# Performance work log

Hardware: AMD Instinct MI355X
Metric: run time of the kernel (lower is better)

Reference implementation:

```python
import jax, jax.numpy as jnp
import numpy as np

K = 1024  # attention hidden dim
H = 1024  # encoder hidden dim


def setup_inputs() -> dict:
    key = jax.random.key(0)
    ks = jax.random.split(key, 8)
    B, S = 32, 2048
    decoder_state = jax.random.normal(ks[0], (B, H), dtype=jnp.float32)
    encoder_hiddens = jax.random.normal(ks[1], (B, S, H), dtype=jnp.float32)
    # Linear params (torch convention: y = x @ W.T + b)
    Wa_w = jax.random.normal(ks[2], (1, K), dtype=jnp.float32) / np.sqrt(K)
    Wa_b = jnp.zeros((1,), dtype=jnp.float32)
    Wb_w = jax.random.normal(ks[3], (K, H), dtype=jnp.float32) / np.sqrt(H)
    Wb_b = jnp.zeros((K,), dtype=jnp.float32)
    Wc_w = jax.random.normal(ks[4], (K, H), dtype=jnp.float32) / np.sqrt(H)
    Wc_b = jnp.zeros((K,), dtype=jnp.float32)
    return {
        "decoder_state": decoder_state,
        "encoder_hiddens": encoder_hiddens,
        "Wa_w": Wa_w, "Wa_b": Wa_b,
        "Wb_w": Wb_w, "Wb_b": Wb_b,
        "Wc_w": Wc_w, "Wc_b": Wc_b,
    }


def reference(decoder_state, encoder_hiddens, Wa_w, Wa_b, Wb_w, Wb_b, Wc_w, Wc_b):
    # dec_proj: [B, K]; enc_proj: [B, S, K]
    dec_proj = decoder_state @ Wb_w.T + Wb_b
    enc_proj = jnp.einsum('bsh,kh->bsk', encoder_hiddens, Wc_w) + Wc_b
    # additive score: tanh then project to scalar -> [B, S]
    e = jnp.tanh(dec_proj[:, None, :] + enc_proj)
    scores = jnp.einsum('bsk,k->bs', e, Wa_w[0]) + Wa_b[0]
    attn = jax.nn.softmax(scores, axis=1)
    # weighted sum over sequence -> [B, H]
    context = jnp.einsum('bs,bsh->bh', attn, encoder_hiddens)
    return context
```

## Files before the change

### kernel.cpp

```cpp
#include <hip/hip_runtime.h>
#include <hip/hip_bf16.h>
#include <stdint.h>

#define B_SZ 32
#define S_SZ 2048
#define H_SZ 1024
#define K_SZ 1024
#define M_SZ (B_SZ * S_SZ)

typedef __attribute__((ext_vector_type(8))) short bf16x8;
typedef __attribute__((ext_vector_type(4))) float f32x4;


__device__ __forceinline__ short f2bf_rne(float f) {
    uint32_t u = __builtin_bit_cast(uint32_t, f);
    u += 0x7fffu + ((u >> 16) & 1u);
    return (short)(u >> 16);
}

__device__ __forceinline__ float bf2f(unsigned short u) {
    return __builtin_bit_cast(float, (uint32_t)u << 16);
}

__device__ __forceinline__ float fast_tanh(float x) {
    float ex = __expf(2.0f * x);
    return 1.0f - 2.0f / (ex + 1.0f);
}


__global__ void cvt_bf16_k(const float* __restrict__ in,
                           __hip_bfloat16* __restrict__ out, int n8) {
    int idx = blockIdx.x * blockDim.x + threadIdx.x;
    int stride = gridDim.x * blockDim.x;
    for (int i = idx; i < n8; i += stride) {
        const float4* p = (const float4*)in + (size_t)i * 2;
        float4 a = p[0], b = p[1];
        bf16x8 r;
        r[0] = f2bf_rne(a.x); r[1] = f2bf_rne(a.y);
        r[2] = f2bf_rne(a.z); r[3] = f2bf_rne(a.w);
        r[4] = f2bf_rne(b.x); r[5] = f2bf_rne(b.y);
        r[6] = f2bf_rne(b.z); r[7] = f2bf_rne(b.w);
        ((bf16x8*)out)[i] = r;
    }
}


__global__ __launch_bounds__(256) void decproj_k(
    const float* __restrict__ ds, const float* __restrict__ Wb,
    const float* __restrict__ Wb_b, const float* __restrict__ Wc_b,
    float* __restrict__ dp) {
    int g = blockIdx.x * 4 + (threadIdx.x >> 6);
    int lane = threadIdx.x & 63;
    int b = g >> 10;
    int k = g & 1023;
    const float4* wrow = (const float4*)(Wb + (size_t)k * H_SZ);
    const float4* xrow = (const float4*)(ds + (size_t)b * H_SZ);
    float sum = 0.f;
#pragma unroll
    for (int it = 0; it < 4; it++) {
        float4 w = wrow[lane + it * 64];
        float4 x = xrow[lane + it * 64];
        sum += w.x * x.x + w.y * x.y + w.z * x.z + w.w * x.w;
    }
#pragma unroll
    for (int off = 1; off < 64; off <<= 1) sum += __shfl_xor(sum, off, 64);
    if (lane == 0) dp[g] = sum + Wb_b[k] + Wc_b[k];
}


template <bool AF32>
__global__ __launch_bounds__(256) void gemm_scores_k(
    const void* __restrict__ Aptr, const __hip_bfloat16* __restrict__ Bw,
    const float* __restrict__ decp, const float* __restrict__ Wa,
    float* __restrict__ sp) {
    constexpr int ABYTES = AF32 ? 128 * 32 * 4 : 128 * 32 * 2;
    __shared__ __align__(16) unsigned char AsmRaw[ABYTES];
    __shared__ __align__(16) unsigned char BsmRaw[128 * 32 * 2];

    const int t = threadIdx.x;
    const int wave = t >> 6;
    const int lane = t & 63;
    const int wm = wave >> 1, wn = wave & 1;
    const int quad = lane >> 4;
    const int l15 = lane & 15;

    const int id = blockIdx.x;
    const int colBlk = (id >> 3) & 7;
    const int rowBlk = ((id >> 6) << 3) | (id & 7);
    const int row0 = rowBlk * 128;
    const int col0 = colBlk * 128;
    const int b = row0 >> 11;

    f32x4 acc[4][4];
#pragma unroll
    for (int i = 0; i < 4; i++)
#pragma unroll
        for (int j = 0; j < 4; j++) acc[i][j] = f32x4{0.f, 0.f, 0.f, 0.f};

    const __hip_bfloat16* Ab = (const __hip_bfloat16*)Aptr;
    const float* Af = (const float*)Aptr;

    for (int k0 = 0; k0 < H_SZ; k0 += 32) {
        if constexpr (AF32) {
#pragma unroll
            for (int inst = 0; inst < 4; inst++) {
                int slot = inst * 256 + t;
                int r = slot >> 3, c4 = slot & 7;
                const float* g = Af + (size_t)(row0 + r) * H_SZ + k0 + c4 * 4;
                __builtin_amdgcn_global_load_lds(
                    (const __attribute__((address_space(1))) void*)g,
                    (__attribute__((address_space(3))) void*)(AsmRaw + inst * 4096 + wave * 1024),
                    16, 0, 0);
            }
        } else {
#pragma unroll
            for (int inst = 0; inst < 2; inst++) {
                int slot = inst * 256 + t;
                int r = slot >> 2, c8 = slot & 3;
                const __hip_bfloat16* g = Ab + (size_t)(row0 + r) * H_SZ + k0 + c8 * 8;
                __builtin_amdgcn_global_load_lds(
                    (const __attribute__((address_space(1))) void*)g,
                    (__attribute__((address_space(3))) void*)(AsmRaw + inst * 4096 + wave * 1024),
                    16, 0, 0);
            }
        }
#pragma unroll
        for (int inst = 0; inst < 2; inst++) {
            int slot = inst * 256 + t;
            int r = slot >> 2, c8 = slot & 3;
            const __hip_bfloat16* g = Bw + (size_t)(col0 + r) * H_SZ + k0 + c8 * 8;
            __builtin_amdgcn_global_load_lds(
                (const __attribute__((address_space(1))) void*)g,
                (__attribute__((address_space(3))) void*)(BsmRaw + inst * 4096 + wave * 1024),
                16, 0, 0);
        }
        __syncthreads();

        bf16x8 afr[4], bfr[4];
#pragma unroll
        for (int i = 0; i < 4; i++) {
            int r = wm * 64 + i * 16 + l15;
            if constexpr (AF32) {
                const float* ap = (const float*)AsmRaw + r * 32 + quad * 8;
                f32x4 lo = *(const f32x4*)ap;
                f32x4 hi = *(const f32x4*)(ap + 4);
                bf16x8 v;
                v[0] = f2bf_rne(lo[0]); v[1] = f2bf_rne(lo[1]);
                v[2] = f2bf_rne(lo[2]); v[3] = f2bf_rne(lo[3]);
                v[4] = f2bf_rne(hi[0]); v[5] = f2bf_rne(hi[1]);
                v[6] = f2bf_rne(hi[2]); v[7] = f2bf_rne(hi[3]);
                afr[i] = v;
            } else {
                afr[i] = *(const bf16x8*)((const __hip_bfloat16*)AsmRaw + r * 32 + quad * 8);
            }
        }
#pragma unroll
        for (int j = 0; j < 4; j++) {
            int r = wn * 64 + j * 16 + l15;
            bfr[j] = *(const bf16x8*)((const __hip_bfloat16*)BsmRaw + r * 32 + quad * 8);
        }
#pragma unroll
        for (int i = 0; i < 4; i++)
#pragma unroll
            for (int j = 0; j < 4; j++)
                acc[i][j] = __builtin_amdgcn_mfma_f32_16x16x32_bf16(afr[i], bfr[j], acc[i][j], 0, 0, 0);
        __syncthreads();
    }

    float wa_j[4], dp_j[4];
#pragma unroll
    for (int j = 0; j < 4; j++) {
        int c = col0 + wn * 64 + j * 16 + l15;
        wa_j[j] = Wa[c];
        dp_j[j] = decp[b * K_SZ + c];
    }
    const int slotIdx = colBlk * 2 + wn;
#pragma unroll
    for (int i = 0; i < 4; i++) {
#pragma unroll
        for (int r = 0; r < 4; r++) {
            float tsum = 0.f;
#pragma unroll
            for (int j = 0; j < 4; j++)
                tsum += wa_j[j] * fast_tanh(acc[i][j][r] + dp_j[j]);
#pragma unroll
            for (int off = 1; off < 16; off <<= 1) tsum += __shfl_xor(tsum, off, 64);
            if (l15 == 0) {
                int m = row0 + wm * 64 + i * 16 + quad * 4 + r;
                sp[(size_t)slotIdx * M_SZ + m] = tsum;
            }
        }
    }
}


__global__ __launch_bounds__(256) void softmax_k(
    const float* __restrict__ sp, float* __restrict__ attn) {
    int b = blockIdx.x;
    int t = threadIdx.x;
    __shared__ float wred[4];
    __shared__ float wred2[4];
    float sc[8];
    float mx = -1e30f;
#pragma unroll
    for (int u = 0; u < 8; u++) {
        int m = b * S_SZ + t + u * 256;
        float v = 0.f;
#pragma unroll
        for (int c = 0; c < 16; c++) v += sp[(size_t)c * M_SZ + m];
        sc[u] = v;
        mx = fmaxf(mx, v);
    }
#pragma unroll
    for (int off = 1; off < 64; off <<= 1) mx = fmaxf(mx, __shfl_xor(mx, off, 64));
    if ((t & 63) == 0) wred[t >> 6] = mx;
    __syncthreads();
    mx = fmaxf(fmaxf(wred[0], wred[1]), fmaxf(wred[2], wred[3]));
    float lsum = 0.f;
#pragma unroll
    for (int u = 0; u < 8; u++) { sc[u] = expf(sc[u] - mx); lsum += sc[u]; }
#pragma unroll
    for (int off = 1; off < 64; off <<= 1) lsum += __shfl_xor(lsum, off, 64);
    if ((t & 63) == 0) wred2[t >> 6] = lsum;
    __syncthreads();
    float inv = 1.f / (wred2[0] + wred2[1] + wred2[2] + wred2[3]);
#pragma unroll
    for (int u = 0; u < 8; u++) attn[b * S_SZ + t + u * 256] = sc[u] * inv;
}


template <bool BF16E>
__global__ __launch_bounds__(256) void ctx_part_k(
    const float* __restrict__ attn, const void* __restrict__ encp,
    float* __restrict__ cp) {
    int b = blockIdx.x >> 5;
    int c = blockIdx.x & 31;
    int t = threadIdx.x;
    __shared__ float wloc[64];
    if (t < 64) wloc[t] = attn[b * S_SZ + c * 64 + t];
    __syncthreads();
    float4 acc = {0.f, 0.f, 0.f, 0.f};
    if constexpr (BF16E) {
        const ushort4* ep = (const ushort4*)((const __hip_bfloat16*)encp +
                              ((size_t)b * S_SZ + (size_t)c * 64) * H_SZ);
#pragma unroll 8
        for (int s = 0; s < 64; s++) {
            float w = wloc[s];
            ushort4 v = ep[s * 256 + t];
            acc.x += w * bf2f(v.x); acc.y += w * bf2f(v.y);
            acc.z += w * bf2f(v.z); acc.w += w * bf2f(v.w);
        }
    } else {
        const float4* ep = (const float4*)((const float*)encp +
                              ((size_t)b * S_SZ + (size_t)c * 64) * H_SZ);
#pragma unroll 8
        for (int s = 0; s < 64; s++) {
            float w = wloc[s];
            float4 v = ep[s * 256 + t];
            acc.x += w * v.x; acc.y += w * v.y;
            acc.z += w * v.z; acc.w += w * v.w;
        }
    }
    ((float4*)(cp + ((size_t)c * B_SZ + b) * H_SZ))[t] = acc;
}

__global__ void ctx_red_k(const float* __restrict__ cp, float* __restrict__ out) {
    int i = blockIdx.x * blockDim.x + threadIdx.x;
    float s = 0.f;
#pragma unroll
    for (int c = 0; c < 32; c++) s += cp[(size_t)c * (B_SZ * H_SZ) + i];
    out[i] = s;
}


extern "C" void kernel_launch(void* const* d_in, const int* in_sizes, int n_in,
                              void* d_out, int out_size, void* d_ws, size_t ws_size,
                              hipStream_t stream) {
    const float* dec  = (const float*)d_in[0];
    const float* enc  = (const float*)d_in[1];
    const float* Wa_w = (const float*)d_in[2];
    const float* Wb_w = (const float*)d_in[4];
    const float* Wb_b = (const float*)d_in[5];
    const float* Wc_w = (const float*)d_in[6];
    const float* Wc_b = (const float*)d_in[7];
    float* out = (float*)d_out;

    char* ws = (char*)d_ws;
    size_t off = 0;
    auto alloc = [&](size_t bytes) -> void* {
        void* p = ws + off;
        off += (bytes + 255) & ~(size_t)255;
        return p;
    };
    __hip_bfloat16* wc_bf = (__hip_bfloat16*)alloc((size_t)K_SZ * H_SZ * 2);
    float* dp     = (float*)alloc((size_t)B_SZ * K_SZ * 4);
    float* spart  = (float*)alloc((size_t)16 * M_SZ * 4);
    float* attn   = (float*)alloc((size_t)B_SZ * S_SZ * 4);
    float* cpart  = (float*)alloc((size_t)32 * B_SZ * H_SZ * 4);
    __hip_bfloat16* enc_bf = (__hip_bfloat16*)alloc((size_t)M_SZ * H_SZ * 2);
    const bool useBf16A = (off <= ws_size);

    cvt_bf16_k<<<512, 256, 0, stream>>>(Wc_w, wc_bf, K_SZ * H_SZ / 8);
    if (useBf16A)
        cvt_bf16_k<<<8192, 256, 0, stream>>>(enc, enc_bf, M_SZ * H_SZ / 8);
    decproj_k<<<8192, 256, 0, stream>>>(dec, Wb_w, Wb_b, Wc_b, dp);
    if (useBf16A)
        gemm_scores_k<false><<<(M_SZ / 128) * 8, 256, 0, stream>>>(enc_bf, wc_bf, dp, Wa_w, spart);
    else
        gemm_scores_k<true><<<(M_SZ / 128) * 8, 256, 0, stream>>>(enc, wc_bf, dp, Wa_w, spart);
    softmax_k<<<B_SZ, 256, 0, stream>>>(spart, attn);
    if (useBf16A)
        ctx_part_k<true><<<B_SZ * 32, 256, 0, stream>>>(attn, enc_bf, cpart);
    else
        ctx_part_k<false><<<B_SZ * 32, 256, 0, stream>>>(attn, enc, cpart);
    ctx_red_k<<<128, 256, 0, stream>>>(cpart, out);
}
```

Baseline: 613.6 us.

## Add 256x256 bf16 MFMA GEMM with async LDS staging for scores

Replaces the 128x128-tile score GEMM on the bf16 path with a 256x256-tile, 512-thread kernel. Its A/B tiles are loaded straight into swizzled LDS with global_load_lds and double-buffered, so the next K-slice loads while the current one computes. Each K tile is split into four phases that interleave LDS fragment reads, async staging and MFMA bursts, with raised wave priority around the MFMAs and explicit vmcnt waits. The larger tile is meant to cut global and LDS traffic per FLOP and hide load latency. In exchange it uses 128KB of LDS per block, which limits occupancy, and its manual barrier/waitcnt scheduling is fragile.

```diff
diff --git a/kernel.cpp b/kernel.cpp
--- a/kernel.cpp
+++ b/kernel.cpp
@@ -65,6 +65,154 @@
 #pragma unroll
     for (int off = 1; off < 64; off <<= 1) sum += __shfl_xor(sum, off, 64);
     if (lane == 0) dp[g] = sum + Wb_b[k] + Wc_b[k];
+}
+
+
+__device__ __forceinline__ void stage_ht(const __hip_bfloat16* __restrict__ src,
+                                         unsigned char* ldsHt, int srcRow0,
+                                         int k0, int t) {
+#pragma unroll
+    for (int inst = 0; inst < 2; inst++) {
+        int slot = inst * 512 + t;
+        int row = slot >> 3;
+        int colB = (slot & 7) << 4;
+        int scol = colB ^ ((row & 7) << 4);
+        const __hip_bfloat16* g = src + (size_t)(srcRow0 + row) * H_SZ + k0 + (scol >> 1);
+        __builtin_amdgcn_global_load_lds(
+            (const __attribute__((address_space(1))) void*)g,
+            (__attribute__((address_space(3))) void*)(ldsHt + inst * 8192 + ((t >> 6) << 10)),
+            16, 0, 0);
+    }
+}
+
+template <int VM, bool SA, bool SB>
+__device__ __forceinline__ void tile_phases(
+    const __hip_bfloat16* __restrict__ Ag, const __hip_bfloat16* __restrict__ Bg,
+    unsigned char* Acur, unsigned char* Bcur, unsigned char* Anxt,
+    int row0, int col0, int kA, int kB, int t,
+    int aRowByte, int bRowByte, int kOff0, int kOff1,
+    f32x4 (&acc)[8][4])
+{
+    bf16x8 bfr[4][2];
+#pragma unroll
+    for (int ph = 0; ph < 4; ++ph) {
+        bf16x8 afr[2][2];
+        if (ph == 0) {
+#pragma unroll
+            for (int n = 0; n < 4; ++n) {
+                bfr[n][0] = *(const bf16x8*)(Bcur + bRowByte + n * 2048 + kOff0);
+                bfr[n][1] = *(const bf16x8*)(Bcur + bRowByte + n * 2048 + kOff1);
+            }
+        }
+#pragma unroll
+        for (int i = 0; i < 2; ++i) {
+            afr[i][0] = *(const bf16x8*)(Acur + aRowByte + (ph * 2 + i) * 2048 + kOff0);
+            afr[i][1] = *(const bf16x8*)(Acur + aRowByte + (ph * 2 + i) * 2048 + kOff1);
+        }
+        if (SA && ph == 0) stage_ht(Ag, Anxt,         row0,       kA, t);
+        if (SA && ph == 1) stage_ht(Ag, Anxt + 16384, row0 + 128, kA, t);
+        if (SB && ph == 2) stage_ht(Bg, Bcur,         col0,       kB, t);
+        if (SB && ph == 3) stage_ht(Bg, Bcur + 16384, col0 + 128, kB, t);
+        __builtin_amdgcn_s_barrier();
+        asm volatile("s_waitcnt lgkmcnt(0)" ::: "memory");
+        __builtin_amdgcn_sched_barrier(0);
+        __builtin_amdgcn_s_setprio(1);
+#pragma unroll
+        for (int i = 0; i < 2; ++i)
+#pragma unroll
+            for (int ks = 0; ks < 2; ++ks)
+#pragma unroll
+                for (int n = 0; n < 4; ++n)
+                    acc[ph * 2 + i][n] = __builtin_amdgcn_mfma_f32_16x16x32_bf16(
+                        afr[i][ks], bfr[n][ks], acc[ph * 2 + i][n], 0, 0, 0);
+        __builtin_amdgcn_s_setprio(0);
+        if (ph == 3 && VM == 4) asm volatile("s_waitcnt vmcnt(4)" ::: "memory");
+        if (ph == 3 && VM == 0) asm volatile("s_waitcnt vmcnt(0)" ::: "memory");
+        __builtin_amdgcn_s_barrier();
+    }
+}
+
+__global__ __launch_bounds__(512, 2) void gemm256_scores_k(
+    const __hip_bfloat16* __restrict__ Ag, const __hip_bfloat16* __restrict__ Bg,
+    const float* __restrict__ decp, const float* __restrict__ Wa,
+    float* __restrict__ sp)
+{
+    __shared__ __align__(16) unsigned char lds[131072];
+    const int t = threadIdx.x;
+    const int wave = t >> 6, lane = t & 63;
+    const int wr = wave >> 2, wc = wave & 3;
+    const int quad = lane >> 4, l15 = lane & 15;
+
+    const int id = blockIdx.x;
+    const int colBlk = (id >> 3) & 3;
+    const int rowBlk = ((id >> 5) << 3) | (id & 7);
+    const int row0 = rowBlk * 256, col0 = colBlk * 256;
+
+    const int swz = (l15 & 7) << 4;
+    const int aRowByte = (wr * 128 + l15) * 128;
+    const int bRowByte = (wc * 64 + l15) * 128;
+    const int kOff0 = (quad * 16) ^ swz;
+    const int kOff1 = (64 + quad * 16) ^ swz;
+
+    f32x4 acc[8][4];
+#pragma unroll
+    for (int i = 0; i < 8; i++)
+#pragma unroll
+        for (int j = 0; j < 4; j++) acc[i][j] = f32x4{0.f, 0.f, 0.f, 0.f};
+
+    unsigned char* A0l = lds;
+    unsigned char* B0l = lds + 32768;
+    unsigned char* A1l = lds + 65536;
+    unsigned char* B1l = lds + 98304;
+
+    stage_ht(Bg, B0l,         col0,       0,  t);
+    stage_ht(Bg, B0l + 16384, col0 + 128, 0,  t);
+    stage_ht(Ag, A0l,         row0,       0,  t);
+    stage_ht(Ag, A0l + 16384, row0 + 128, 0,  t);
+    stage_ht(Bg, B1l,         col0,       64, t);
+    stage_ht(Bg, B1l + 16384, col0 + 128, 64, t);
+    asm volatile("s_waitcnt vmcnt(4)" ::: "memory");
+    __builtin_amdgcn_s_barrier();
+
+#pragma unroll 2
+    for (int tt = 0; tt < 14; ++tt) {
+        unsigned char* Ac = (tt & 1) ? A1l : A0l;
+        unsigned char* Bc = (tt & 1) ? B1l : B0l;
+        unsigned char* An = (tt & 1) ? A0l : A1l;
+        tile_phases<4, true, true>(Ag, Bg, Ac, Bc, An, row0, col0,
+                                   (tt + 1) * 64, (tt + 2) * 64, t,
+                                   aRowByte, bRowByte, kOff0, kOff1, acc);
+    }
+    tile_phases<0, true, false>(Ag, Bg, A0l, B0l, A1l, row0, col0,
+                                15 * 64, 0, t, aRowByte, bRowByte, kOff0, kOff1, acc);
+    tile_phases<-1, false, false>(Ag, Bg, A1l, B1l, A0l, row0, col0,
+                                  0, 0, t, aRowByte, bRowByte, kOff0, kOff1, acc);
+
+    const int b = row0 >> 11;
+    float wa_j[4], dp_j[4];
+#pragma unroll
+    for (int n = 0; n < 4; ++n) {
+        int c = col0 + wc * 64 + n * 16 + l15;
+        wa_j[n] = Wa[c];
+        dp_j[n] = decp[b * K_SZ + c];
+    }
+    const int slotIdx = colBlk * 4 + wc;
+#pragma unroll
+    for (int m = 0; m < 8; ++m) {
+#pragma unroll
+        for (int r = 0; r < 4; ++r) {
+            float tsum = 0.f;
+#pragma unroll
+            for (int n = 0; n < 4; ++n)
+                tsum += wa_j[n] * fast_tanh(acc[m][n][r] + dp_j[n]);
+#pragma unroll
+            for (int off = 1; off < 16; off <<= 1) tsum += __shfl_xor(tsum, off, 64);
+            if (l15 == 0) {
+                int mrow = row0 + wr * 128 + m * 16 + quad * 4 + r;
+                sp[(size_t)slotIdx * M_SZ + mrow] = tsum;
+            }
+        }
+    }
 }
 
 
@@ -305,7 +453,7 @@
         cvt_bf16_k<<<8192, 256, 0, stream>>>(enc, enc_bf, M_SZ * H_SZ / 8);
     decproj_k<<<8192, 256, 0, stream>>>(dec, Wb_w, Wb_b, Wc_b, dp);
     if (useBf16A)
-        gemm_scores_k<false><<<(M_SZ / 128) * 8, 256, 0, stream>>>(enc_bf, wc_bf, dp, Wa_w, spart);
+        gemm256_scores_k<<<(M_SZ / 256) * (K_SZ / 256), 512, 0, stream>>>(enc_bf, wc_bf, dp, Wa_w, spart);
     else
         gemm_scores_k<true><<<(M_SZ / 128) * 8, 256, 0, stream>>>(enc, wc_bf, dp, Wa_w, spart);
     softmax_k<<<B_SZ, 256, 0, stream>>>(spart, attn);
```

Result: faster. 568.7 us (-7.3%).
